# Optimization experiments

Hardware: AMD Instinct MI355X
Metric: run time of the kernel (lower is better)

Reference implementation:

```python
import jax, jax.numpy as jnp
import numpy as np

N = 10000      # nodes
DEG = 32       # avg degree
D_IN = 256     # in_feats
H = 128        # hidden_layers[0] == hidden_layers[2]
K = 3          # hidden_layers[1] = Chebyshev order
D_OUT = 64     # out_feat


def setup_inputs() -> dict:
    key = jax.random.key(0)
    ks = jax.random.split(key, 8)
    x = jax.random.normal(ks[0], (N, D_IN), jnp.float32)
    # sparse binary adjacency built by scattering into a dense [N, N] matrix
    src = jax.random.randint(ks[1], (N * DEG,), 0, N)
    dst = jax.random.randint(ks[2], (N * DEG,), 0, N)
    adj = jnp.zeros((N, N), jnp.float32).at[src, dst].set(1.0)
    init = lambda k, shape, fan: jax.random.normal(k, shape, jnp.float32) / np.sqrt(fan)
    W_in = init(ks[3], (D_IN, H), D_IN)
    b_in = jnp.zeros((H,), jnp.float32)
    W_cheb = init(ks[4], (K * H, H), K * H)   # dgl ChebConv: Linear(k*in, out)
    b_cheb = jnp.zeros((H,), jnp.float32)
    W_out = init(ks[5], (H, D_OUT), H)
    b_out = jnp.zeros((D_OUT,), jnp.float32)
    return dict(x=x, adj=adj, W_in=W_in, b_in=b_in, W_cheb=W_cheb,
                b_cheb=b_cheb, W_out=W_out, b_out=b_out)


def reference(x, adj, W_in, b_in, W_cheb, b_cheb, W_out, b_out):
    n = x.shape[0]
    # graph construction from dense adjacency (eager, like adj.to_dense().nonzero())
    src, dst = jnp.nonzero(adj)
    # symmetric normalization on in-degrees (dgl ChebConv, norm clamped at 1)
    deg = jax.ops.segment_sum(jnp.ones(src.shape[0], jnp.float32), dst, num_segments=n)
    norm = jnp.clip(deg, 1.0) ** -0.5  # [n]
    re_norm = 2.0 / 2.0  # lambda_max = [2] -> re_norm = 1

    def prop(h):
        # D^{-1/2} A D^{-1/2} h : gather at src, scatter-add at dst
        return jax.ops.segment_sum((h * norm[:, None])[src], dst, num_segments=n) * norm[:, None]

    # input linear + relu
    h = jax.nn.relu(x @ W_in + b_in)
    # Chebyshev recursion (dgl ChebConv with lambda_max=2)
    X0 = h
    X1 = -re_norm * prop(X0) + (re_norm - 1.0) * X0
    Xs = [X0, X1]
    Xpp, Xp = X0, X1
    for _ in range(2, K):
        Xi = -2.0 * re_norm * prop(Xp) + 2.0 * (re_norm - 1.0) * Xp - Xpp
        Xs.append(Xi)
        Xpp, Xp = Xp, Xi
    hc = jax.nn.relu(jnp.concatenate(Xs, axis=1) @ W_cheb + b_cheb)  # [n, H]
    return hc @ W_out + b_out  # [n, D_OUT]
```

## Files before the change

### kernel.cpp

```cpp
#include <hip/hip_runtime.h>
#include <hip/hip_bf16.h>
#include <cstdint>
#include <cstddef>

#define NN 10000
#define MAXDEG 128
#define LDX 384

#define GEMM_BLKS 313
#define SCAN_BLKS 2048
#define FAT_BLKS  (GEMM_BLKS + 1 + SCAN_BLKS)
#define SEG 256
#define NWAVES (SCAN_BLKS * 4)

typedef __attribute__((ext_vector_type(8))) short bf16x8;
typedef __attribute__((ext_vector_type(4))) float f32x4;

__device__ __forceinline__ float bf2f(unsigned short u) {
    union { unsigned int i; float f; } c; c.i = ((unsigned int)u) << 16; return c.f;
}
__device__ __forceinline__ unsigned short f2bf(float f) {
    union { float f; unsigned int i; } c; c.f = f;
    unsigned int x = c.i;
    return (unsigned short)((x + 0x7fffu + ((x >> 16) & 1u)) >> 16);
}

__device__ __forceinline__ void scan_compact(float4 v, int p, int lane,
                                             unsigned int* __restrict__ myseg,
                                             int& base) {
    unsigned m = (v.x != 0.f ? 1u : 0u) | (v.y != 0.f ? 2u : 0u)
               | (v.z != 0.f ? 4u : 0u) | (v.w != 0.f ? 8u : 0u);
    #pragma unroll
    for (int c = 0; c < 4; ++c) {
        unsigned long long bal = __ballot((m >> c) & 1u);
        if (bal) {
            if ((m >> c) & 1u) {
                int off = (int)__popcll(bal & ((1ull << lane) - 1ull));
                int l = p * 4 + c;
                int i = l / NN;
                int j = l - i * NN;
                if (base + off < SEG)
                    myseg[base + off] = (unsigned)((j << 14) | i);
            }
            base += (int)__popcll(bal);
        }
    }
}

__global__ __launch_bounds__(256) void fat_scan_gemm(
        const float4* __restrict__ adj4, int total4,
        unsigned int* __restrict__ edges, int* __restrict__ waveCnt,
        int* __restrict__ cnt,
        const float* __restrict__ x, const float* __restrict__ W_in,
        const float* __restrict__ b_in,
        const float* __restrict__ W_cheb, const float* __restrict__ W_out,
        unsigned short* __restrict__ Xc,
        unsigned short* __restrict__ Wtc, unsigned short* __restrict__ Wto) {
    __shared__ float smem[5120];
    int bid = blockIdx.x;
    int t = threadIdx.x;

    if (bid < GEMM_BLKS) {
        constexpr int K = 256, N = 128, BM = 32, KC = 32;
        float* Wl = smem;
        float* Al = smem + KC * N;
        int r0 = bid * BM;
        int c2 = t & 63;
        int g  = t >> 6;
        float2 acc[8];
        #pragma unroll
        for (int i = 0; i < 8; ++i) acc[i] = make_float2(0.f, 0.f);

        for (int kk = 0; kk < K; kk += KC) {
            __syncthreads();
            #pragma unroll
            for (int i = 0; i < KC * N / 4 / 256; ++i) {
                int idx = t + i * 256;
                ((float4*)Wl)[idx] = ((const float4*)(W_in + (size_t)kk * N))[idx];
            }
            {
                int row = t >> 3;
                int cf  = t & 7;
                float4 v = make_float4(0.f, 0.f, 0.f, 0.f);
                if (r0 + row < NN)
                    v = *(const float4*)(x + (size_t)(r0 + row) * K + kk + cf * 4);
                *(float4*)(Al + row * KC + cf * 4) = v;
            }
            __syncthreads();
            for (int k = 0; k < KC; k += 4) {
                float4 av[8];
                #pragma unroll
                for (int rr = 0; rr < 8; ++rr)
                    av[rr] = *(const float4*)(Al + (g * 8 + rr) * KC + k);
                #pragma unroll
                for (int k2 = 0; k2 < 4; ++k2) {
                    float2 wv = *(const float2*)(Wl + (k + k2) * N + c2 * 2);
                    #pragma unroll
                    for (int rr = 0; rr < 8; ++rr) {
                        float a = (k2 == 0) ? av[rr].x : (k2 == 1) ? av[rr].y
                                  : (k2 == 2) ? av[rr].z : av[rr].w;
                        acc[rr].x = fmaf(a, wv.x, acc[rr].x);
                        acc[rr].y = fmaf(a, wv.y, acc[rr].y);
                    }
                }
            }
        }
        float2 bv = *(const float2*)(b_in + c2 * 2);
        #pragma unroll
        for (int rr = 0; rr < 8; ++rr) {
            int r = r0 + g * 8 + rr;
            if (r < NN) {
                float vx = fmaxf(acc[rr].x + bv.x, 0.f);
                float vy = fmaxf(acc[rr].y + bv.y, 0.f);
                uint32_t o = (uint32_t)f2bf(vx) | ((uint32_t)f2bf(vy) << 16);
                *(uint32_t*)(Xc + (size_t)r * LDX + c2 * 2) = o;
            }
        }
    } else if (bid == GEMM_BLKS) {
        for (int idx = t; idx < 384 * 128; idx += 256) {
            int k = idx >> 7, c = idx & 127;
            Wtc[c * 384 + k] = f2bf(W_cheb[idx]);
        }
        for (int idx = t; idx < 128 * 64; idx += 256) {
            int k = idx >> 6, c = idx & 63;
            Wto[c * 128 + k] = f2bf(W_out[idx]);
        }
        for (int idx = t; idx < NN; idx += 256) cnt[idx] = 0;
    } else {
        int sid = bid - (GEMM_BLKS + 1);
        int w = t >> 6, lane = t & 63;
        int wid = sid * 4 + w;
        unsigned int* myseg = edges + (size_t)wid * SEG;
        int base = 0;

        int stride = SCAN_BLKS * 256;
        int p0 = sid * 256 + t;
        const float4 Z = make_float4(0.f, 0.f, 0.f, 0.f);
        int iters = (total4 + 2 * stride - 1) / (2 * stride);

        int pa = p0, pb = p0 + stride;
        float4 va = (pa < total4) ? adj4[pa] : Z;
        float4 vb = (pb < total4) ? adj4[pb] : Z;
        int pc = p0 + 2 * stride, pd = p0 + 3 * stride;
        float4 vc = (pc < total4) ? adj4[pc] : Z;
        float4 vd = (pd < total4) ? adj4[pd] : Z;

        for (int it = 0; it < iters; ++it) {
            int pe = p0 + (2 * it + 4) * stride;
            int pf = p0 + (2 * it + 5) * stride;
            float4 ve = (it + 2 < iters && pe < total4) ? adj4[pe] : Z;
            float4 vf = (it + 2 < iters && pf < total4) ? adj4[pf] : Z;
            int p = p0 + (2 * it) * stride;
            scan_compact(va, p, lane, myseg, base);
            scan_compact(vb, p + stride, lane, myseg, base);
            va = vc; vb = vd; vc = ve; vd = vf;
        }
        if (lane == 0) waveCnt[wid] = (base < SEG) ? base : SEG;
    }
}

__global__ __launch_bounds__(256) void csr_build(const unsigned int* __restrict__ edges,
                                                 const int* __restrict__ waveCnt,
                                                 int* __restrict__ cnt,
                                                 int* __restrict__ csr) {
    int wid = blockIdx.x * 4 + (threadIdx.x >> 6);
    int lane = threadIdx.x & 63;
    int n = waveCnt[wid];
    const unsigned int* seg = edges + (size_t)wid * SEG;
    for (int e = lane; e < n; e += 64) {
        unsigned u = seg[e];
        int i = (int)(u & 16383u);
        int j = (int)(u >> 14);
        int pos = atomicAdd(&cnt[j], 1);
        if (pos < MAXDEG) csr[j * MAXDEG + pos] = i;
    }
}

template<bool SUB>
__global__ __launch_bounds__(256) void prop_k(unsigned short* __restrict__ X,
                                              const int* __restrict__ csr,
                                              const int* __restrict__ cnt,
                                              int srcOff, int dstOff, float scale) {
    int j = blockIdx.x * 4 + (threadIdx.x >> 6);
    if (j >= NN) return;
    int lane = threadIdx.x & 63;
    int cj = cnt[j];
    int cn = min(cj, MAXDEG);
    const int* nb = csr + j * MAXDEG;
    float ax0 = 0.f, ay0 = 0.f, ax1 = 0.f, ay1 = 0.f;
    int e = 0;
    for (; e + 2 <= cn; e += 2) {
        int i0 = nb[e], i1 = nb[e + 1];
        int c0 = cnt[i0], c1 = cnt[i1];
        uint32_t h0 = *(const uint32_t*)(X + (size_t)i0 * LDX + srcOff + lane * 2);
        uint32_t h1 = *(const uint32_t*)(X + (size_t)i1 * LDX + srcOff + lane * 2);
        float w0 = rsqrtf(fmaxf((float)c0, 1.f));
        float w1 = rsqrtf(fmaxf((float)c1, 1.f));
        ax0 = fmaf(w0, bf2f((unsigned short)h0), ax0);
        ay0 = fmaf(w0, bf2f((unsigned short)(h0 >> 16)), ay0);
        ax1 = fmaf(w1, bf2f((unsigned short)h1), ax1);
        ay1 = fmaf(w1, bf2f((unsigned short)(h1 >> 16)), ay1);
    }
    if (e < cn) {
        int i0 = nb[e];
        float w0 = rsqrtf(fmaxf((float)cnt[i0], 1.f));
        uint32_t h0 = *(const uint32_t*)(X + (size_t)i0 * LDX + srcOff + lane * 2);
        ax0 = fmaf(w0, bf2f((unsigned short)h0), ax0);
        ay0 = fmaf(w0, bf2f((unsigned short)(h0 >> 16)), ay0);
    }
    float s = scale * rsqrtf(fmaxf((float)cj, 1.f));
    float rx = s * (ax0 + ax1), ry = s * (ay0 + ay1);
    if (SUB) {
        uint32_t x0 = *(const uint32_t*)(X + (size_t)j * LDX + lane * 2);
        rx -= bf2f((unsigned short)x0);
        ry -= bf2f((unsigned short)(x0 >> 16));
    }
    uint32_t o = (uint32_t)f2bf(rx) | ((uint32_t)f2bf(ry) << 16);
    *(uint32_t*)(X + (size_t)j * LDX + dstOff + lane * 2) = o;
}

__global__ __launch_bounds__(256) void cheb_out_mfma(
        const unsigned short* __restrict__ Xc,
        const unsigned short* __restrict__ Wtc,
        const float* __restrict__ bc,
        const unsigned short* __restrict__ Wto,
        const float* __restrict__ bo,
        float* __restrict__ out) {
    __shared__ unsigned short hcL[32][136];
    int t = threadIdx.x;
    int w = t >> 6, lane = t & 63;
    int r0 = blockIdx.x * 32;
    int lr = lane & 15;
    int kg = lane >> 4;

    f32x4 acc[2][2] = {};
    for (int k0 = 0; k0 < 384; k0 += 32) {
        bf16x8 a[2], b[2];
        #pragma unroll
        for (int m = 0; m < 2; ++m) {
            int row = r0 + m * 16 + lr;
            row = min(row, NN - 1);
            a[m] = *(const bf16x8*)(Xc + (size_t)row * LDX + k0 + kg * 8);
        }
        #pragma unroll
        for (int n = 0; n < 2; ++n) {
            int col = w * 32 + n * 16 + lr;
            b[n] = *(const bf16x8*)(Wtc + (size_t)col * 384 + k0 + kg * 8);
        }
        #pragma unroll
        for (int m = 0; m < 2; ++m)
            #pragma unroll
            for (int n = 0; n < 2; ++n)
                acc[m][n] = __builtin_amdgcn_mfma_f32_16x16x32_bf16(a[m], b[n], acc[m][n], 0, 0, 0);
    }
    #pragma unroll
    for (int m = 0; m < 2; ++m) {
        #pragma unroll
        for (int n = 0; n < 2; ++n) {
            int col = w * 32 + n * 16 + lr;
            float bv = bc[col];
            #pragma unroll
            for (int r = 0; r < 4; ++r) {
                int row = m * 16 + kg * 4 + r;
                hcL[row][col] = f2bf(fmaxf(acc[m][n][r] + bv, 0.f));
            }
        }
    }
    __syncthreads();
    int rt = w >> 1, ch = w & 1;
    f32x4 a2[2] = {};
    for (int k0 = 0; k0 < 128; k0 += 32) {
        bf16x8 af = *(const bf16x8*)(&hcL[rt * 16 + lr][k0 + kg * 8]);
        #pragma unroll
        for (int n = 0; n < 2; ++n) {
            int col = ch * 32 + n * 16 + lr;
            bf16x8 bf_ = *(const bf16x8*)(Wto + (size_t)col * 128 + k0 + kg * 8);
            a2[n] = __builtin_amdgcn_mfma_f32_16x16x32_bf16(af, bf_, a2[n], 0, 0, 0);
        }
    }
    #pragma unroll
    for (int n = 0; n < 2; ++n) {
        int col = ch * 32 + n * 16 + lr;
        float bv = bo[col];
        #pragma unroll
        for (int r = 0; r < 4; ++r) {
            int row = r0 + rt * 16 + kg * 4 + r;
            if (row < NN) out[(size_t)row * 64 + col] = a2[n][r] + bv;
        }
    }
}

extern "C" void kernel_launch(void* const* d_in, const int* in_sizes, int n_in,
                              void* d_out, int out_size, void* d_ws, size_t ws_size,
                              hipStream_t stream) {
    const float* x      = (const float*)d_in[0];
    const float* adj    = (const float*)d_in[1];
    const float* W_in   = (const float*)d_in[2];
    const float* b_in   = (const float*)d_in[3];
    const float* W_cheb = (const float*)d_in[4];
    const float* b_cheb = (const float*)d_in[5];
    const float* W_out  = (const float*)d_in[6];
    const float* b_out  = (const float*)d_in[7];
    float* out = (float*)d_out;

    char* ws = (char*)d_ws;
    int*            cnt     = (int*)(ws + 0);
    int*            waveCnt = (int*)(ws + 40960);
    int*            csr     = (int*)(ws + 73728);
    unsigned int*   edges   = (unsigned int*)(ws + 5193728);
    unsigned short* Xc      = (unsigned short*)(ws + 13582336);
    unsigned short* Wtc     = (unsigned short*)(ws + 21262336);
    unsigned short* Wto     = (unsigned short*)(ws + 21360640);

    int adj_total = in_sizes[1];

    fat_scan_gemm<<<FAT_BLKS, 256, 0, stream>>>(
        (const float4*)adj, adj_total / 4, edges, waveCnt, cnt,
        x, W_in, b_in, W_cheb, W_out, Xc, Wtc, Wto);
    csr_build<<<SCAN_BLKS, 256, 0, stream>>>(edges, waveCnt, cnt, csr);
    prop_k<false><<<(NN + 3) / 4, 256, 0, stream>>>(Xc, csr, cnt, 0, 128, -1.0f);
    prop_k<true><<<(NN + 3) / 4, 256, 0, stream>>>(Xc, csr, cnt, 128, 256, -2.0f);
    cheb_out_mfma<<<(NN + 31) / 32, 256, 0, stream>>>(Xc, Wtc, b_cheb, Wto, b_out, out);
}
```

Measured before the change: 224.4 us.

## Scan adjacency in contiguous per-block regions with deeper prefetch; unroll prop by four

The dense adjacency scan now gives each of 1018 blocks a contiguous 24576-float4 region instead of a grid-stride loop over 2048 blocks. It keeps an 8-deep register prefetch buffer and skips the ballot work when a wave sees no nonzeros. Scan blocks are placed first in the grid ahead of the GEMM and weight-prep blocks, so the bandwidth-bound scan starts earlier. The propagation kernel gathers four neighbours per iteration instead of two for more memory-level parallelism, and csr_build gets a bounds guard for the new wave count. The risks are higher register pressure and a fixed per-block region size that must match the input size.

```diff
diff --git a/kernel.cpp b/kernel.cpp
--- a/kernel.cpp
+++ b/kernel.cpp
@@ -7,9 +7,10 @@
 #define MAXDEG 128
 #define LDX 384
 
+#define SCAN_BLKS 1018
+#define SREG 24576
 #define GEMM_BLKS 313
-#define SCAN_BLKS 2048
-#define FAT_BLKS  (GEMM_BLKS + 1 + SCAN_BLKS)
+#define FAT_BLKS (SCAN_BLKS + 1 + GEMM_BLKS)
 #define SEG 256
 #define NWAVES (SCAN_BLKS * 4)
 
@@ -23,28 +24,6 @@
     union { float f; unsigned int i; } c; c.f = f;
     unsigned int x = c.i;
     return (unsigned short)((x + 0x7fffu + ((x >> 16) & 1u)) >> 16);
-}
-
-__device__ __forceinline__ void scan_compact(float4 v, int p, int lane,
-                                             unsigned int* __restrict__ myseg,
-                                             int& base) {
-    unsigned m = (v.x != 0.f ? 1u : 0u) | (v.y != 0.f ? 2u : 0u)
-               | (v.z != 0.f ? 4u : 0u) | (v.w != 0.f ? 8u : 0u);
-    #pragma unroll
-    for (int c = 0; c < 4; ++c) {
-        unsigned long long bal = __ballot((m >> c) & 1u);
-        if (bal) {
-            if ((m >> c) & 1u) {
-                int off = (int)__popcll(bal & ((1ull << lane) - 1ull));
-                int l = p * 4 + c;
-                int i = l / NN;
-                int j = l - i * NN;
-                if (base + off < SEG)
-                    myseg[base + off] = (unsigned)((j << 14) | i);
-            }
-            base += (int)__popcll(bal);
-        }
-    }
 }
 
 __global__ __launch_bounds__(256) void fat_scan_gemm(
@@ -60,11 +39,63 @@
     int bid = blockIdx.x;
     int t = threadIdx.x;
 
-    if (bid < GEMM_BLKS) {
+    if (bid < SCAN_BLKS) {
+        int w = t >> 6, lane = t & 63;
+        int wid = bid * 4 + w;
+        unsigned int* myseg = edges + (size_t)wid * SEG;
+        int base = 0;
+        int p0 = bid * SREG + t;
+        int LIM = total4 - 1;
+
+        float4 buf[8];
+        #pragma unroll
+        for (int d = 0; d < 8; ++d)
+            buf[d] = adj4[min(p0 + d * 256, LIM)];
+
+        for (int g = 0; g < 96; g += 8) {
+            #pragma unroll
+            for (int d = 0; d < 8; ++d) {
+                int p = p0 + (g + d) * 256;
+                float4 v = buf[d];
+                buf[d] = adj4[min(p + 8 * 256, LIM)];
+                unsigned m = (v.x != 0.f ? 1u : 0u) | (v.y != 0.f ? 2u : 0u)
+                           | (v.z != 0.f ? 4u : 0u) | (v.w != 0.f ? 8u : 0u);
+                if (p > LIM) m = 0;
+                if (__any((int)m)) {
+                    #pragma unroll
+                    for (int c = 0; c < 4; ++c) {
+                        unsigned long long bal = __ballot((m >> c) & 1u);
+                        if (bal) {
+                            if ((m >> c) & 1u) {
+                                int off = (int)__popcll(bal & ((1ull << lane) - 1ull));
+                                int l = p * 4 + c;
+                                int i = l / NN;
+                                int j = l - i * NN;
+                                if (base + off < SEG)
+                                    myseg[base + off] = (unsigned)((j << 14) | i);
+                            }
+                            base += (int)__popcll(bal);
+                        }
+                    }
+                }
+            }
+        }
+        if (lane == 0) waveCnt[wid] = (base < SEG) ? base : SEG;
+    } else if (bid == SCAN_BLKS) {
+        for (int idx = t; idx < 384 * 128; idx += 256) {
+            int k = idx >> 7, c = idx & 127;
+            Wtc[c * 384 + k] = f2bf(W_cheb[idx]);
+        }
+        for (int idx = t; idx < 128 * 64; idx += 256) {
+            int k = idx >> 6, c = idx & 63;
+            Wto[c * 128 + k] = f2bf(W_out[idx]);
+        }
+        for (int idx = t; idx < NN; idx += 256) cnt[idx] = 0;
+    } else {
         constexpr int K = 256, N = 128, BM = 32, KC = 32;
         float* Wl = smem;
         float* Al = smem + KC * N;
-        int r0 = bid * BM;
+        int r0 = (bid - SCAN_BLKS - 1) * BM;
         int c2 = t & 63;
         int g  = t >> 6;
         float2 acc[8];
@@ -116,46 +147,6 @@
                 *(uint32_t*)(Xc + (size_t)r * LDX + c2 * 2) = o;
             }
         }
-    } else if (bid == GEMM_BLKS) {
-        for (int idx = t; idx < 384 * 128; idx += 256) {
-            int k = idx >> 7, c = idx & 127;
-            Wtc[c * 384 + k] = f2bf(W_cheb[idx]);
-        }
-        for (int idx = t; idx < 128 * 64; idx += 256) {
-            int k = idx >> 6, c = idx & 63;
-            Wto[c * 128 + k] = f2bf(W_out[idx]);
-        }
-        for (int idx = t; idx < NN; idx += 256) cnt[idx] = 0;
-    } else {
-        int sid = bid - (GEMM_BLKS + 1);
-        int w = t >> 6, lane = t & 63;
-        int wid = sid * 4 + w;
-        unsigned int* myseg = edges + (size_t)wid * SEG;
-        int base = 0;
-
-        int stride = SCAN_BLKS * 256;
-        int p0 = sid * 256 + t;
-        const float4 Z = make_float4(0.f, 0.f, 0.f, 0.f);
-        int iters = (total4 + 2 * stride - 1) / (2 * stride);
-
-        int pa = p0, pb = p0 + stride;
-        float4 va = (pa < total4) ? adj4[pa] : Z;
-        float4 vb = (pb < total4) ? adj4[pb] : Z;
-        int pc = p0 + 2 * stride, pd = p0 + 3 * stride;
-        float4 vc = (pc < total4) ? adj4[pc] : Z;
-        float4 vd = (pd < total4) ? adj4[pd] : Z;
-
-        for (int it = 0; it < iters; ++it) {
-            int pe = p0 + (2 * it + 4) * stride;
-            int pf = p0 + (2 * it + 5) * stride;
-            float4 ve = (it + 2 < iters && pe < total4) ? adj4[pe] : Z;
-            float4 vf = (it + 2 < iters && pf < total4) ? adj4[pf] : Z;
-            int p = p0 + (2 * it) * stride;
-            scan_compact(va, p, lane, myseg, base);
-            scan_compact(vb, p + stride, lane, myseg, base);
-            va = vc; vb = vd; vc = ve; vd = vf;
-        }
-        if (lane == 0) waveCnt[wid] = (base < SEG) ? base : SEG;
     }
 }
 
@@ -165,6 +156,7 @@
                                                  int* __restrict__ csr) {
     int wid = blockIdx.x * 4 + (threadIdx.x >> 6);
     int lane = threadIdx.x & 63;
+    if (wid >= NWAVES) return;
     int n = waveCnt[wid];
     const unsigned int* seg = edges + (size_t)wid * SEG;
     for (int e = lane; e < n; e += 64) {
@@ -188,20 +180,29 @@
     int cn = min(cj, MAXDEG);
     const int* nb = csr + j * MAXDEG;
     float ax0 = 0.f, ay0 = 0.f, ax1 = 0.f, ay1 = 0.f;
+    float ax2 = 0.f, ay2 = 0.f, ax3 = 0.f, ay3 = 0.f;
     int e = 0;
-    for (; e + 2 <= cn; e += 2) {
-        int i0 = nb[e], i1 = nb[e + 1];
-        int c0 = cnt[i0], c1 = cnt[i1];
+    for (; e + 4 <= cn; e += 4) {
+        int i0 = nb[e], i1 = nb[e + 1], i2 = nb[e + 2], i3 = nb[e + 3];
+        int c0 = cnt[i0], c1 = cnt[i1], c2 = cnt[i2], c3 = cnt[i3];
         uint32_t h0 = *(const uint32_t*)(X + (size_t)i0 * LDX + srcOff + lane * 2);
         uint32_t h1 = *(const uint32_t*)(X + (size_t)i1 * LDX + srcOff + lane * 2);
+        uint32_t h2 = *(const uint32_t*)(X + (size_t)i2 * LDX + srcOff + lane * 2);
+        uint32_t h3 = *(const uint32_t*)(X + (size_t)i3 * LDX + srcOff + lane * 2);
         float w0 = rsqrtf(fmaxf((float)c0, 1.f));
         float w1 = rsqrtf(fmaxf((float)c1, 1.f));
+        float w2 = rsqrtf(fmaxf((float)c2, 1.f));
+        float w3 = rsqrtf(fmaxf((float)c3, 1.f));
         ax0 = fmaf(w0, bf2f((unsigned short)h0), ax0);
         ay0 = fmaf(w0, bf2f((unsigned short)(h0 >> 16)), ay0);
         ax1 = fmaf(w1, bf2f((unsigned short)h1), ax1);
         ay1 = fmaf(w1, bf2f((unsigned short)(h1 >> 16)), ay1);
-    }
-    if (e < cn) {
+        ax2 = fmaf(w2, bf2f((unsigned short)h2), ax2);
+        ay2 = fmaf(w2, bf2f((unsigned short)(h2 >> 16)), ay2);
+        ax3 = fmaf(w3, bf2f((unsigned short)h3), ax3);
+        ay3 = fmaf(w3, bf2f((unsigned short)(h3 >> 16)), ay3);
+    }
+    for (; e < cn; ++e) {
         int i0 = nb[e];
         float w0 = rsqrtf(fmaxf((float)cnt[i0], 1.f));
         uint32_t h0 = *(const uint32_t*)(X + (size_t)i0 * LDX + srcOff + lane * 2);
@@ -209,7 +210,8 @@
         ay0 = fmaf(w0, bf2f((unsigned short)(h0 >> 16)), ay0);
     }
     float s = scale * rsqrtf(fmaxf((float)cj, 1.f));
-    float rx = s * (ax0 + ax1), ry = s * (ay0 + ay1);
+    float rx = s * ((ax0 + ax1) + (ax2 + ax3));
+    float ry = s * ((ay0 + ay1) + (ay2 + ay3));
     if (SUB) {
         uint32_t x0 = *(const uint32_t*)(X + (size_t)j * LDX + lane * 2);
         rx -= bf2f((unsigned short)x0);
```

Result: slower. 229.9 us (+2.4%).
